# Kernel optimization log

Measured on AMD Instinct MI355X. Metric: run time of the kernel, lower is better.

Reference implementation:

```python
import jax, jax.numpy as jnp
import numpy as np

B, P, C, D, H = 32, 2048, 19, 512, 4
DH = D // H  # 128
EPS = 1e-5


def setup_inputs() -> dict:
    key = jax.random.key(0)
    ks = jax.random.split(key, 12)
    s = 0.02
    return {
        "x": jax.random.normal(ks[0], (B, P, D), jnp.float32),
        "channel_embeddings": jax.random.normal(ks[1], (C, D), jnp.float32),
        "Wq": jax.random.normal(ks[2], (D, D), jnp.float32) * s,
        "bq": jnp.zeros((D,), jnp.float32),
        "Wk": jax.random.normal(ks[3], (D, D), jnp.float32) * s,
        "bk": jnp.zeros((D,), jnp.float32),
        "Wv": jax.random.normal(ks[4], (D, D), jnp.float32) * s,
        "bv": jnp.zeros((D,), jnp.float32),
        "Wo": jax.random.normal(ks[5], (D, D), jnp.float32) * s,
        "bo": jnp.zeros((D,), jnp.float32),
        "gamma": jnp.ones((D,), jnp.float32),
        "beta": jnp.zeros((D,), jnp.float32),
    }


def reference(x, channel_embeddings, Wq, bq, Wk, bk, Wv, bv, Wo, bo, gamma, beta):
    # q: (B, P, H, DH)
    q = (x @ Wq.T + bq).reshape(B, P, H, DH)
    # K/V depend only on channel embeddings (same for every batch/patch in the
    # original; it merely materialized the broadcast). Compute once: (C, H, DH)
    k = (channel_embeddings @ Wk.T + bk).reshape(C, H, DH)
    v = (channel_embeddings @ Wv.T + bv).reshape(C, H, DH)
    # scores over channels: (B, P, C, H)
    scores = jnp.einsum("bphd,chd->bpch", q, k) / jnp.sqrt(jnp.float32(DH))
    weights = jax.nn.softmax(scores, axis=2)  # softmax over channel dim
    # weighted sum of channel values: (B, P, H, DH) -> (B, P, D)
    attended = jnp.einsum("bpch,chd->bphd", weights, v).reshape(B, P, D)
    out = attended @ Wo.T + bo  # dropout is identity in eval mode
    # residual + layernorm
    h = x + out
    mean = jnp.mean(h, axis=-1, keepdims=True)
    var = jnp.mean(jnp.square(h - mean), axis=-1, keepdims=True)
    return (h - mean) * jax.lax.rsqrt(var + EPS) * gamma + beta
```

## Files before the change

### kernel.cpp

```cpp
#include <hip/hip_runtime.h>
#include <hip/hip_bf16.h>

#define C_  19
#define D_  512
#define H_  4
#define DH_ 128
#define NROW 65536
#define CHP_ 96

typedef float f32x4 __attribute__((ext_vector_type(4)));
typedef short bf16x8 __attribute__((ext_vector_type(8)));

__device__ __forceinline__ unsigned short f2bf(float f) {
  union { __hip_bfloat16 h; unsigned short s; } u;
  u.h = __float2bfloat16(f);
  return u.s;
}
__device__ __forceinline__ float bf2f(unsigned short h) {
  return __uint_as_float(((unsigned int)h) << 16);
}
__device__ __forceinline__ bf16x8 ld_cvt8(const float* p) {
  f32x4 v0 = *(const f32x4*)p;
  f32x4 v1 = *(const f32x4*)(p + 4);
  bf16x8 a;
  a[0]=(short)f2bf(v0[0]); a[1]=(short)f2bf(v0[1]);
  a[2]=(short)f2bf(v0[2]); a[3]=(short)f2bf(v0[3]);
  a[4]=(short)f2bf(v1[0]); a[5]=(short)f2bf(v1[1]);
  a[6]=(short)f2bf(v1[2]); a[7]=(short)f2bf(v1[3]);
  return a;
}

__global__ __launch_bounds__(512) void prep(
    const float* __restrict__ ce,
    const float* __restrict__ Wq, const float* __restrict__ bq,
    const float* __restrict__ Wk, const float* __restrict__ bk,
    const float* __restrict__ Wv, const float* __restrict__ bv,
    const float* __restrict__ Wo, const float* __restrict__ bo,
    unsigned short* __restrict__ Mtf, unsigned short* __restrict__ Utf,
    float* __restrict__ s0g)
{
  __shared__ float KV[2][DH_];
  __shared__ float KVp[512];

  const int p = blockIdx.x;
  const int m = threadIdx.x;
  const int mt_off = (p>>4)*8192 + (m>>5)*512 + ((((m>>3)&3)<<4) + (p&15))*8 + (m&7);
  const int ut_off = ((m>>4)*3 + (p>>5))*512 + ((((p>>3)&3)<<4) + (m&15))*8 + (p&7);
  const int c = p >> 2, h = p & 3;

  if (c >= C_) {
    if (p < 80) { Mtf[mt_off] = 0; if (m == 0) s0g[p] = 0.f; }
    Utf[ut_off] = (p == 80) ? f2bf(bo[m]) : (unsigned short)0;
    return;
  }

  {
    const int which = m >> 8;
    const int dh    = (m >> 1) & 127;
    const int half  = m & 1;
    const float* w = (which ? Wv : Wk) + (size_t)(h*DH_ + dh)*D_ + half*256;
    const float* e = ce + (size_t)c*D_ + half*256;
    float acc = 0.f;
    #pragma unroll 8
    for (int d = 0; d < 256; ++d) acc = fmaf(e[d], w[d], acc);
    KVp[m] = acc;
  }
  __syncthreads();
  if (m < 256) {
    const int which = m >> 7, dh = m & 127;
    KV[which][dh] = KVp[2*m] + KVp[2*m+1] + (which ? bv : bk)[h*DH_ + dh];
  }
  __syncthreads();

  const float rs128 = 0.08838834764831843f;
  float macc = 0.f;
  #pragma unroll 4
  for (int dh = 0; dh < DH_; ++dh)
    macc = fmaf(Wq[(size_t)(h*DH_+dh)*D_ + m], KV[0][dh], macc);
  Mtf[mt_off] = f2bf(macc * rs128);

  float uacc = 0.f;
  const float* wor = Wo + (size_t)m*D_ + h*DH_;
  #pragma unroll 4
  for (int dh = 0; dh < DH_; ++dh)
    uacc = fmaf(wor[dh], KV[1][dh], uacc);
  Utf[ut_off] = f2bf(uacc);

  if (m == 0) {
    float sa = 0.f;
    for (int dh = 0; dh < DH_; ++dh) sa = fmaf(bq[h*DH_+dh], KV[0][dh], sa);
    s0g[p] = sa * rs128;
  }
}

__global__ __launch_bounds__(64, 2) void fused16w(
    const float* __restrict__ x,
    const unsigned short* __restrict__ Mtf,
    const unsigned short* __restrict__ Utf,
    const float* __restrict__ s0g,
    const float* __restrict__ gamma, const float* __restrict__ beta,
    float* __restrict__ out)
{
  __shared__ __attribute__((aligned(16))) unsigned short Xbf[16*512];
  __shared__ __attribute__((aligned(16))) unsigned short WaL[16][104];

  const int lane = threadIdx.x;
  const int lhi  = lane >> 4;
  const int llo  = lane & 15;
  const int row0 = blockIdx.x * 16;

  #pragma unroll
  for (int j = 0; j < 16; ++j) {
    bf16x8 a = ld_cvt8(x + (size_t)(row0 + j)*D_ + lane*8);
    int byteoff = j*1024 + ((lane*16) ^ ((j & 7) << 4));
    *(bf16x8*)((char*)Xbf + byteoff) = a;
  }
  asm volatile("s_waitcnt lgkmcnt(0)" ::: "memory");
  __builtin_amdgcn_sched_barrier(0);

  {
    const char* xb = (const char*)Xbf + llo*1024;
    const int swz = (llo & 7) << 4;
    f32x4 acc0 = (f32x4){0,0,0,0}, acc1 = acc0, acc2 = acc0, acc3 = acc0, acc4 = acc0;
    #pragma unroll
    for (int ks = 0; ks < 16; ++ks) {
      bf16x8 a = *(const bf16x8*)(xb + ((ks*64 + lhi*16) ^ swz));
      acc0 = __builtin_amdgcn_mfma_f32_16x16x32_bf16(a, *(const bf16x8*)(Mtf + 0*8192 + ks*512 + lane*8), acc0, 0, 0, 0);
      acc1 = __builtin_amdgcn_mfma_f32_16x16x32_bf16(a, *(const bf16x8*)(Mtf + 1*8192 + ks*512 + lane*8), acc1, 0, 0, 0);
      acc2 = __builtin_amdgcn_mfma_f32_16x16x32_bf16(a, *(const bf16x8*)(Mtf + 2*8192 + ks*512 + lane*8), acc2, 0, 0, 0);
      acc3 = __builtin_amdgcn_mfma_f32_16x16x32_bf16(a, *(const bf16x8*)(Mtf + 3*8192 + ks*512 + lane*8), acc3, 0, 0, 0);
      acc4 = __builtin_amdgcn_mfma_f32_16x16x32_bf16(a, *(const bf16x8*)(Mtf + 4*8192 + ks*512 + lane*8), acc4, 0, 0, 0);
    }
    const bool dead = (llo >= 12);
    float s0v0 = s0g[llo], s0v1 = s0g[16+llo], s0v2 = s0g[32+llo],
          s0v3 = s0g[48+llo], s0v4 = s0g[64+llo];
    #pragma unroll
    for (int r = 0; r < 4; ++r) {
      float v0 = acc0[r] + s0v0;
      float v1 = acc1[r] + s0v1;
      float v2 = acc2[r] + s0v2;
      float v3 = acc3[r] + s0v3;
      float v4 = dead ? -1e30f : (acc4[r] + s0v4);
      float mx = fmaxf(fmaxf(fmaxf(v0, v1), fmaxf(v2, v3)), v4);
      mx = fmaxf(mx, __shfl_xor(mx, 4, 64));
      mx = fmaxf(mx, __shfl_xor(mx, 8, 64));
      float e0 = __expf(v0 - mx), e1 = __expf(v1 - mx), e2 = __expf(v2 - mx),
            e3 = __expf(v3 - mx), e4 = dead ? 0.f : __expf(v4 - mx);
      float sm = e0 + e1 + e2 + e3 + e4;
      sm += __shfl_xor(sm, 4, 64);
      sm += __shfl_xor(sm, 8, 64);
      float inv = 1.f / sm;
      int lr = lhi*4 + r;
      WaL[lr][     llo] = f2bf(e0 * inv);
      WaL[lr][16 + llo] = f2bf(e1 * inv);
      WaL[lr][32 + llo] = f2bf(e2 * inv);
      WaL[lr][48 + llo] = f2bf(e3 * inv);
      WaL[lr][64 + llo] = f2bf(e4 * inv);
    }
    {
      int prow = lhi*4 + (llo & 3);
      int cj   = llo >> 2;
      unsigned short v0 = (cj == 0) ? (unsigned short)0x3F80 : (unsigned short)0;
      WaL[prow][80 + cj*4 + 0] = v0;
      WaL[prow][80 + cj*4 + 1] = 0;
      WaL[prow][80 + cj*4 + 2] = 0;
      WaL[prow][80 + cj*4 + 3] = 0;
    }
  }
  asm volatile("s_waitcnt lgkmcnt(0)" ::: "memory");
  __builtin_amdgcn_sched_barrier(0);

  f32x4 oacc[32];
  #pragma unroll
  for (int i = 0; i < 32; ++i) oacc[i] = (f32x4){0.f,0.f,0.f,0.f};
  #pragma unroll
  for (int ks = 0; ks < 3; ++ks) {
    bf16x8 a = *(const bf16x8*)&WaL[llo][ks*32 + lhi*8];
    #pragma unroll
    for (int t = 0; t < 32; ++t) {
      bf16x8 b = *(const bf16x8*)(Utf + (size_t)(t*3 + ks)*512 + lane*8);
      oacc[t] = __builtin_amdgcn_mfma_f32_16x16x32_bf16(a, b, oacc[t], 0, 0, 0);
    }
  }

  float s[4] = {0,0,0,0}, q[4] = {0,0,0,0};
  #pragma unroll
  for (int t = 0; t < 32; ++t) {
    int n = t*16 + llo;
    #pragma unroll
    for (int r = 0; r < 4; ++r) {
      int mr = lhi*4 + r;
      float xres = bf2f(*(const unsigned short*)
          ((const char*)Xbf + mr*1024 + ((n*2) ^ ((mr & 7) << 4))));
      float val = oacc[t][r] + xres;
      oacc[t][r] = val;
      s[r] += val;
      q[r] = fmaf(val, val, q[r]);
    }
  }
  #pragma unroll
  for (int r = 0; r < 4; ++r) {
    #pragma unroll
    for (int off = 1; off < 16; off <<= 1) {
      s[r] += __shfl_xor(s[r], off, 64);
      q[r] += __shfl_xor(q[r], off, 64);
    }
  }
  float mu_r[4], rstd_r[4];
  #pragma unroll
  for (int r = 0; r < 4; ++r) {
    float mu  = s[r] * (1.f/(float)D_);
    float var = q[r] * (1.f/(float)D_) - mu*mu;
    mu_r[r]   = mu;
    rstd_r[r] = rsqrtf(var + 1e-5f);
  }
  #pragma unroll
  for (int t = 0; t < 32; ++t) {
    int n = t*16 + llo;
    float g = gamma[n], bt = beta[n];
    #pragma unroll
    for (int r = 0; r < 4; ++r) {
      out[(size_t)(row0 + lhi*4 + r)*D_ + n] = (oacc[t][r] - mu_r[r]) * rstd_r[r] * g + bt;
    }
  }
}

extern "C" void kernel_launch(void* const* d_in, const int* in_sizes, int n_in,
                              void* d_out, int out_size, void* d_ws, size_t ws_size,
                              hipStream_t stream) {
  const float* x     = (const float*)d_in[0];
  const float* ce    = (const float*)d_in[1];
  const float* Wq    = (const float*)d_in[2];
  const float* bq    = (const float*)d_in[3];
  const float* Wk    = (const float*)d_in[4];
  const float* bk    = (const float*)d_in[5];
  const float* Wv    = (const float*)d_in[6];
  const float* bv    = (const float*)d_in[7];
  const float* Wo    = (const float*)d_in[8];
  const float* bo    = (const float*)d_in[9];
  const float* gamma = (const float*)d_in[10];
  const float* beta  = (const float*)d_in[11];
  float* out = (float*)d_out;

  char* ws = (char*)d_ws;
  unsigned short* Mtf = (unsigned short*)(ws);
  unsigned short* Utf = (unsigned short*)(ws + 81920);
  float* s0g          = (float*)(ws + 180224);

  prep<<<CHP_, 512, 0, stream>>>(ce, Wq, bq, Wk, bk, Wv, bv, Wo, bo,
                                 Mtf, Utf, s0g);
  fused16w<<<NROW/16, 64, 0, stream>>>(x, Mtf, Utf, s0g, gamma, beta, out);
}
```

Baseline: 140.1 us.

## Restructure fused kernel into 256-row blocks with LDS-staged Utf and transposed score MFMA

Each block now handles 256 rows with 8 waves, and Utf is staged once per block into LDS. The score GEMM is transposed so x is read straight from global into registers, with each wave covering 32 rows. The residual is re-read from global memory in fp32 instead of the bf16 LDS copy. This aims to cut repeated global loads of Utf and raise per-block reuse, but it uses about 150KB of LDS per block, which limits occupancy. The second x read may add memory traffic if it misses cache.

```diff
diff --git a/kernel.cpp b/kernel.cpp
--- a/kernel.cpp
+++ b/kernel.cpp
@@ -7,6 +7,7 @@
 #define DH_ 128
 #define NROW 65536
 #define CHP_ 96
+#define WPITCH 104
 
 typedef float f32x4 __attribute__((ext_vector_type(4)));
 typedef short bf16x8 __attribute__((ext_vector_type(8)));
@@ -15,9 +16,6 @@
   union { __hip_bfloat16 h; unsigned short s; } u;
   u.h = __float2bfloat16(f);
   return u.s;
-}
-__device__ __forceinline__ float bf2f(unsigned short h) {
-  return __uint_as_float(((unsigned int)h) << 16);
 }
 __device__ __forceinline__ bf16x8 ld_cvt8(const float* p) {
   f32x4 v0 = *(const f32x4*)p;
@@ -93,7 +91,7 @@
   }
 }
 
-__global__ __launch_bounds__(64, 2) void fused16w(
+__global__ __launch_bounds__(512, 2) void fused256(
     const float* __restrict__ x,
     const unsigned short* __restrict__ Mtf,
     const unsigned short* __restrict__ Utf,
@@ -101,126 +99,136 @@
     const float* __restrict__ gamma, const float* __restrict__ beta,
     float* __restrict__ out)
 {
-  __shared__ __attribute__((aligned(16))) unsigned short Xbf[16*512];
-  __shared__ __attribute__((aligned(16))) unsigned short WaL[16][104];
-
-  const int lane = threadIdx.x;
+  __shared__ __attribute__((aligned(16))) unsigned short UtfL[CHP_*512];
+  __shared__ __attribute__((aligned(16))) unsigned short WaL[256][WPITCH];
+
+  const int t    = threadIdx.x;
+  const int w    = t >> 6;
+  const int lane = t & 63;
   const int lhi  = lane >> 4;
   const int llo  = lane & 15;
-  const int row0 = blockIdx.x * 16;
+  const int row0 = blockIdx.x * 256;
+  const int wr   = w * 32;
 
   #pragma unroll
-  for (int j = 0; j < 16; ++j) {
-    bf16x8 a = ld_cvt8(x + (size_t)(row0 + j)*D_ + lane*8);
-    int byteoff = j*1024 + ((lane*16) ^ ((j & 7) << 4));
-    *(bf16x8*)((char*)Xbf + byteoff) = a;
-  }
-  asm volatile("s_waitcnt lgkmcnt(0)" ::: "memory");
-  __builtin_amdgcn_sched_barrier(0);
-
+  for (int i = 0; i < 12; ++i) {
+    int off = i*8192 + t*16;
+    *(bf16x8*)((char*)UtfL + off) = *(const bf16x8*)((const char*)Utf + off);
+  }
+
+  f32x4 acc[5][2];
+  #pragma unroll
+  for (int m = 0; m < 5; ++m)
+    #pragma unroll
+    for (int j = 0; j < 2; ++j) acc[m][j] = (f32x4){0,0,0,0};
   {
-    const char* xb = (const char*)Xbf + llo*1024;
-    const int swz = (llo & 7) << 4;
-    f32x4 acc0 = (f32x4){0,0,0,0}, acc1 = acc0, acc2 = acc0, acc3 = acc0, acc4 = acc0;
+    const float* xr0 = x + (size_t)(row0 + wr      + llo)*D_ + lhi*8;
+    const float* xr1 = x + (size_t)(row0 + wr + 16 + llo)*D_ + lhi*8;
     #pragma unroll
     for (int ks = 0; ks < 16; ++ks) {
-      bf16x8 a = *(const bf16x8*)(xb + ((ks*64 + lhi*16) ^ swz));
-      acc0 = __builtin_amdgcn_mfma_f32_16x16x32_bf16(a, *(const bf16x8*)(Mtf + 0*8192 + ks*512 + lane*8), acc0, 0, 0, 0);
-      acc1 = __builtin_amdgcn_mfma_f32_16x16x32_bf16(a, *(const bf16x8*)(Mtf + 1*8192 + ks*512 + lane*8), acc1, 0, 0, 0);
-      acc2 = __builtin_amdgcn_mfma_f32_16x16x32_bf16(a, *(const bf16x8*)(Mtf + 2*8192 + ks*512 + lane*8), acc2, 0, 0, 0);
-      acc3 = __builtin_amdgcn_mfma_f32_16x16x32_bf16(a, *(const bf16x8*)(Mtf + 3*8192 + ks*512 + lane*8), acc3, 0, 0, 0);
-      acc4 = __builtin_amdgcn_mfma_f32_16x16x32_bf16(a, *(const bf16x8*)(Mtf + 4*8192 + ks*512 + lane*8), acc4, 0, 0, 0);
-    }
-    const bool dead = (llo >= 12);
-    float s0v0 = s0g[llo], s0v1 = s0g[16+llo], s0v2 = s0g[32+llo],
-          s0v3 = s0g[48+llo], s0v4 = s0g[64+llo];
+      bf16x8 xb0 = ld_cvt8(xr0 + ks*32);
+      bf16x8 xb1 = ld_cvt8(xr1 + ks*32);
+      #pragma unroll
+      for (int m = 0; m < 5; ++m) {
+        bf16x8 a = *(const bf16x8*)(Mtf + m*8192 + ks*512 + lane*8);
+        acc[m][0] = __builtin_amdgcn_mfma_f32_16x16x32_bf16(a, xb0, acc[m][0], 0, 0, 0);
+        acc[m][1] = __builtin_amdgcn_mfma_f32_16x16x32_bf16(a, xb1, acc[m][1], 0, 0, 0);
+      }
+    }
+  }
+
+  {
+    const bool dead = (lhi == 3);
+    #pragma unroll
+    for (int t2 = 0; t2 < 2; ++t2) {
+      #pragma unroll
+      for (int r = 0; r < 4; ++r) {
+        float v0 = acc[0][t2][r] + s0g[ 0 + lhi*4 + r];
+        float v1 = acc[1][t2][r] + s0g[16 + lhi*4 + r];
+        float v2 = acc[2][t2][r] + s0g[32 + lhi*4 + r];
+        float v3 = acc[3][t2][r] + s0g[48 + lhi*4 + r];
+        float v4 = dead ? -1e30f : (acc[4][t2][r] + s0g[64 + lhi*4 + r]);
+        float mx = fmaxf(fmaxf(fmaxf(v0, v1), fmaxf(v2, v3)), v4);
+        mx = fmaxf(mx, __shfl_xor(mx, 16, 64));
+        mx = fmaxf(mx, __shfl_xor(mx, 32, 64));
+        float e0 = __expf(v0 - mx), e1 = __expf(v1 - mx), e2 = __expf(v2 - mx),
+              e3 = __expf(v3 - mx), e4 = dead ? 0.f : __expf(v4 - mx);
+        float sm = e0 + e1 + e2 + e3 + e4;
+        sm += __shfl_xor(sm, 16, 64);
+        sm += __shfl_xor(sm, 32, 64);
+        float inv = 1.f / sm;
+        int xr = wr + t2*16 + llo;
+        WaL[xr][ 0 + lhi*4 + r] = f2bf(e0 * inv);
+        WaL[xr][16 + lhi*4 + r] = f2bf(e1 * inv);
+        WaL[xr][32 + lhi*4 + r] = f2bf(e2 * inv);
+        WaL[xr][48 + lhi*4 + r] = f2bf(e3 * inv);
+        WaL[xr][64 + lhi*4 + r] = f2bf(e4 * inv);
+      }
+    }
+    {
+      int rr = wr + (lane & 31);
+      int cb = 80 + (lane >> 5) * 8;
+      bf16x8 z = (bf16x8){0,0,0,0,0,0,0,0};
+      if (cb == 80) z[0] = (short)0x3F80;
+      *(bf16x8*)&WaL[rr][cb] = z;
+    }
+  }
+  __syncthreads();
+
+  #pragma unroll 1
+  for (int pp = 0; pp < 2; ++pp) {
+    const int base = wr + pp*16;
+    f32x4 oacc[32];
+    #pragma unroll
+    for (int i = 0; i < 32; ++i) oacc[i] = (f32x4){0,0,0,0};
+    #pragma unroll
+    for (int ks = 0; ks < 3; ++ks) {
+      bf16x8 a = *(const bf16x8*)&WaL[base + llo][ks*32 + lhi*8];
+      #pragma unroll
+      for (int tl = 0; tl < 32; ++tl) {
+        bf16x8 b = *(const bf16x8*)((const char*)UtfL + (size_t)(tl*3 + ks)*1024 + lane*16);
+        oacc[tl] = __builtin_amdgcn_mfma_f32_16x16x32_bf16(a, b, oacc[tl], 0, 0, 0);
+      }
+    }
+
+    float s[4] = {0,0,0,0}, q[4] = {0,0,0,0};
+    #pragma unroll
+    for (int tl = 0; tl < 32; ++tl) {
+      int n = tl*16 + llo;
+      #pragma unroll
+      for (int r = 0; r < 4; ++r) {
+        int mr = base + lhi*4 + r;
+        float val = oacc[tl][r] + x[(size_t)(row0 + mr)*D_ + n];
+        oacc[tl][r] = val;
+        s[r] += val;
+        q[r] = fmaf(val, val, q[r]);
+      }
+    }
     #pragma unroll
     for (int r = 0; r < 4; ++r) {
-      float v0 = acc0[r] + s0v0;
-      float v1 = acc1[r] + s0v1;
-      float v2 = acc2[r] + s0v2;
-      float v3 = acc3[r] + s0v3;
-      float v4 = dead ? -1e30f : (acc4[r] + s0v4);
-      float mx = fmaxf(fmaxf(fmaxf(v0, v1), fmaxf(v2, v3)), v4);
-      mx = fmaxf(mx, __shfl_xor(mx, 4, 64));
-      mx = fmaxf(mx, __shfl_xor(mx, 8, 64));
-      float e0 = __expf(v0 - mx), e1 = __expf(v1 - mx), e2 = __expf(v2 - mx),
-            e3 = __expf(v3 - mx), e4 = dead ? 0.f : __expf(v4 - mx);
-      float sm = e0 + e1 + e2 + e3 + e4;
-      sm += __shfl_xor(sm, 4, 64);
-      sm += __shfl_xor(sm, 8, 64);
-      float inv = 1.f / sm;
-      int lr = lhi*4 + r;
-      WaL[lr][     llo] = f2bf(e0 * inv);
-      WaL[lr][16 + llo] = f2bf(e1 * inv);
-      WaL[lr][32 + llo] = f2bf(e2 * inv);
-      WaL[lr][48 + llo] = f2bf(e3 * inv);
-      WaL[lr][64 + llo] = f2bf(e4 * inv);
-    }
-    {
-      int prow = lhi*4 + (llo & 3);
-      int cj   = llo >> 2;
-      unsigned short v0 = (cj == 0) ? (unsigned short)0x3F80 : (unsigned short)0;
-      WaL[prow][80 + cj*4 + 0] = v0;
-      WaL[prow][80 + cj*4 + 1] = 0;
-      WaL[prow][80 + cj*4 + 2] = 0;
-      WaL[prow][80 + cj*4 + 3] = 0;
-    }
-  }
-  asm volatile("s_waitcnt lgkmcnt(0)" ::: "memory");
-  __builtin_amdgcn_sched_barrier(0);
-
-  f32x4 oacc[32];
-  #pragma unroll
-  for (int i = 0; i < 32; ++i) oacc[i] = (f32x4){0.f,0.f,0.f,0.f};
-  #pragma unroll
-  for (int ks = 0; ks < 3; ++ks) {
-    bf16x8 a = *(const bf16x8*)&WaL[llo][ks*32 + lhi*8];
-    #pragma unroll
-    for (int t = 0; t < 32; ++t) {
-      bf16x8 b = *(const bf16x8*)(Utf + (size_t)(t*3 + ks)*512 + lane*8);
-      oacc[t] = __builtin_amdgcn_mfma_f32_16x16x32_bf16(a, b, oacc[t], 0, 0, 0);
-    }
-  }
-
-  float s[4] = {0,0,0,0}, q[4] = {0,0,0,0};
-  #pragma unroll
-  for (int t = 0; t < 32; ++t) {
-    int n = t*16 + llo;
+      #pragma unroll
+      for (int off = 1; off < 16; off <<= 1) {
+        s[r] += __shfl_xor(s[r], off, 64);
+        q[r] += __shfl_xor(q[r], off, 64);
+      }
+    }
+    float mu_r[4], rstd_r[4];
     #pragma unroll
     for (int r = 0; r < 4; ++r) {
-      int mr = lhi*4 + r;
-      float xres = bf2f(*(const unsigned short*)
-          ((const char*)Xbf + mr*1024 + ((n*2) ^ ((mr & 7) << 4))));
-      float val = oacc[t][r] + xres;
-      oacc[t][r] = val;
-      s[r] += val;
-      q[r] = fmaf(val, val, q[r]);
-    }
-  }
-  #pragma unroll
-  for (int r = 0; r < 4; ++r) {
-    #pragma unroll
-    for (int off = 1; off < 16; off <<= 1) {
-      s[r] += __shfl_xor(s[r], off, 64);
-      q[r] += __shfl_xor(q[r], off, 64);
-    }
-  }
-  float mu_r[4], rstd_r[4];
-  #pragma unroll
-  for (int r = 0; r < 4; ++r) {
-    float mu  = s[r] * (1.f/(float)D_);
-    float var = q[r] * (1.f/(float)D_) - mu*mu;
-    mu_r[r]   = mu;
-    rstd_r[r] = rsqrtf(var + 1e-5f);
-  }
-  #pragma unroll
-  for (int t = 0; t < 32; ++t) {
-    int n = t*16 + llo;
-    float g = gamma[n], bt = beta[n];
-    #pragma unroll
-    for (int r = 0; r < 4; ++r) {
-      out[(size_t)(row0 + lhi*4 + r)*D_ + n] = (oacc[t][r] - mu_r[r]) * rstd_r[r] * g + bt;
+      float mu  = s[r] * (1.f/(float)D_);
+      float var = q[r] * (1.f/(float)D_) - mu*mu;
+      mu_r[r]   = mu;
+      rstd_r[r] = rsqrtf(var + 1e-5f);
+    }
+    #pragma unroll
+    for (int tl = 0; tl < 32; ++tl) {
+      int n = tl*16 + llo;
+      float g = gamma[n], bt = beta[n];
+      #pragma unroll
+      for (int r = 0; r < 4; ++r) {
+        int mr = base + lhi*4 + r;
+        out[(size_t)(row0 + mr)*D_ + n] = (oacc[tl][r] - mu_r[r]) * rstd_r[r] * g + bt;
+      }
     }
   }
 }
@@ -249,5 +257,5 @@
 
   prep<<<CHP_, 512, 0, stream>>>(ce, Wq, bq, Wk, bk, Wv, bv, Wo, bo,
                                  Mtf, Utf, s0g);
-  fused16w<<<NROW/16, 64, 0, stream>>>(x, Mtf, Utf, s0g, gamma, beta, out);
-}
+  fused256<<<NROW/256, 512, 0, stream>>>(x, Mtf, Utf, s0g, gamma, beta, out);
+}
```

After: 156.8 us. +12.0%, slower.

## Drop LDS x staging, split output GEMM into halves to raise occupancy

Applied to the files above, without the earlier changes.

Removes the 16 KB LDS staging of x and loads the MFMA A-operand straight from global memory, converting to bf16 in registers. The output GEMM is split into two 256-column halves, and the first half's residual-added values are stashed in registers as packed bf16. This halves the accumulator register footprint so the launch bound can allow 4 waves per SIMD instead of 2. In exchange, x is read from global twice (projection and residual), and the first half's pre-LayerNorm values lose precision through bf16 packing.

```diff
diff --git a/kernel.cpp b/kernel.cpp
--- a/kernel.cpp
+++ b/kernel.cpp
@@ -93,7 +93,7 @@
   }
 }
 
-__global__ __launch_bounds__(64, 2) void fused16w(
+__global__ __launch_bounds__(64, 4) void fused16s(
     const float* __restrict__ x,
     const unsigned short* __restrict__ Mtf,
     const unsigned short* __restrict__ Utf,
@@ -101,7 +101,6 @@
     const float* __restrict__ gamma, const float* __restrict__ beta,
     float* __restrict__ out)
 {
-  __shared__ __attribute__((aligned(16))) unsigned short Xbf[16*512];
   __shared__ __attribute__((aligned(16))) unsigned short WaL[16][104];
 
   const int lane = threadIdx.x;
@@ -109,22 +108,12 @@
   const int llo  = lane & 15;
   const int row0 = blockIdx.x * 16;
 
-  #pragma unroll
-  for (int j = 0; j < 16; ++j) {
-    bf16x8 a = ld_cvt8(x + (size_t)(row0 + j)*D_ + lane*8);
-    int byteoff = j*1024 + ((lane*16) ^ ((j & 7) << 4));
-    *(bf16x8*)((char*)Xbf + byteoff) = a;
-  }
-  asm volatile("s_waitcnt lgkmcnt(0)" ::: "memory");
-  __builtin_amdgcn_sched_barrier(0);
-
   {
-    const char* xb = (const char*)Xbf + llo*1024;
-    const int swz = (llo & 7) << 4;
     f32x4 acc0 = (f32x4){0,0,0,0}, acc1 = acc0, acc2 = acc0, acc3 = acc0, acc4 = acc0;
+    const float* xr = x + (size_t)(row0 + llo)*D_ + lhi*8;
     #pragma unroll
     for (int ks = 0; ks < 16; ++ks) {
-      bf16x8 a = *(const bf16x8*)(xb + ((ks*64 + lhi*16) ^ swz));
+      bf16x8 a = ld_cvt8(xr + ks*32);
       acc0 = __builtin_amdgcn_mfma_f32_16x16x32_bf16(a, *(const bf16x8*)(Mtf + 0*8192 + ks*512 + lane*8), acc0, 0, 0, 0);
       acc1 = __builtin_amdgcn_mfma_f32_16x16x32_bf16(a, *(const bf16x8*)(Mtf + 1*8192 + ks*512 + lane*8), acc1, 0, 0, 0);
       acc2 = __builtin_amdgcn_mfma_f32_16x16x32_bf16(a, *(const bf16x8*)(Mtf + 2*8192 + ks*512 + lane*8), acc2, 0, 0, 0);
@@ -160,8 +149,7 @@
     {
       int prow = lhi*4 + (llo & 3);
       int cj   = llo >> 2;
-      unsigned short v0 = (cj == 0) ? (unsigned short)0x3F80 : (unsigned short)0;
-      WaL[prow][80 + cj*4 + 0] = v0;
+      WaL[prow][80 + cj*4 + 0] = (cj == 0) ? (unsigned short)0x3F80 : (unsigned short)0;
       WaL[prow][80 + cj*4 + 1] = 0;
       WaL[prow][80 + cj*4 + 2] = 0;
       WaL[prow][80 + cj*4 + 3] = 0;
@@ -170,34 +158,59 @@
   asm volatile("s_waitcnt lgkmcnt(0)" ::: "memory");
   __builtin_amdgcn_sched_barrier(0);
 
-  f32x4 oacc[32];
-  #pragma unroll
-  for (int i = 0; i < 32; ++i) oacc[i] = (f32x4){0.f,0.f,0.f,0.f};
+  float s[4] = {0,0,0,0}, q[4] = {0,0,0,0};
+  unsigned int pk[32];
+  f32x4 oa[16];
+
+  #pragma unroll
+  for (int i = 0; i < 16; ++i) oa[i] = (f32x4){0,0,0,0};
   #pragma unroll
   for (int ks = 0; ks < 3; ++ks) {
-    bf16x8 a = *(const bf16x8*)&WaL[llo][ks*32 + lhi*8];
-    #pragma unroll
-    for (int t = 0; t < 32; ++t) {
-      bf16x8 b = *(const bf16x8*)(Utf + (size_t)(t*3 + ks)*512 + lane*8);
-      oacc[t] = __builtin_amdgcn_mfma_f32_16x16x32_bf16(a, b, oacc[t], 0, 0, 0);
-    }
-  }
-
-  float s[4] = {0,0,0,0}, q[4] = {0,0,0,0};
-  #pragma unroll
-  for (int t = 0; t < 32; ++t) {
-    int n = t*16 + llo;
+    bf16x8 aw = *(const bf16x8*)&WaL[llo][ks*32 + lhi*8];
+    #pragma unroll
+    for (int tl = 0; tl < 16; ++tl) {
+      bf16x8 b = *(const bf16x8*)(Utf + (size_t)(tl*3 + ks)*512 + lane*8);
+      oa[tl] = __builtin_amdgcn_mfma_f32_16x16x32_bf16(aw, b, oa[tl], 0, 0, 0);
+    }
+  }
+  #pragma unroll
+  for (int tl = 0; tl < 16; ++tl) {
+    int n = tl*16 + llo;
     #pragma unroll
     for (int r = 0; r < 4; ++r) {
-      int mr = lhi*4 + r;
-      float xres = bf2f(*(const unsigned short*)
-          ((const char*)Xbf + mr*1024 + ((n*2) ^ ((mr & 7) << 4))));
-      float val = oacc[t][r] + xres;
-      oacc[t][r] = val;
+      float val = oa[tl][r] + x[(size_t)(row0 + lhi*4 + r)*D_ + n];
+      oa[tl][r] = val;
       s[r] += val;
       q[r] = fmaf(val, val, q[r]);
     }
-  }
+    pk[tl*2    ] = (unsigned int)f2bf(oa[tl][0]) | ((unsigned int)f2bf(oa[tl][1]) << 16);
+    pk[tl*2 + 1] = (unsigned int)f2bf(oa[tl][2]) | ((unsigned int)f2bf(oa[tl][3]) << 16);
+  }
+
+  #pragma unroll
+  for (int i = 0; i < 16; ++i) oa[i] = (f32x4){0,0,0,0};
+  #pragma unroll
+  for (int ks = 0; ks < 3; ++ks) {
+    bf16x8 aw = *(const bf16x8*)&WaL[llo][ks*32 + lhi*8];
+    #pragma unroll
+    for (int tl = 0; tl < 16; ++tl) {
+      bf16x8 b = *(const bf16x8*)(Utf + (size_t)((16 + tl)*3 + ks)*512 + lane*8);
+      oa[tl] = __builtin_amdgcn_mfma_f32_16x16x32_bf16(aw, b, oa[tl], 0, 0, 0);
+    }
+  }
+  #pragma unroll
+  for (int tl = 0; tl < 16; ++tl) {
+    int n = 256 + tl*16 + llo;
+    #pragma unroll
+    for (int r = 0; r < 4; ++r) {
+      float val = oa[tl][r] + x[(size_t)(row0 + lhi*4 + r)*D_ + n];
+      oa[tl][r] = val;
+      s[r] += val;
+      q[r] = fmaf(val, val, q[r]);
+    }
+  }
+
+  float mu_r[4], rstd_r[4];
   #pragma unroll
   for (int r = 0; r < 4; ++r) {
     #pragma unroll
@@ -205,23 +218,33 @@
       s[r] += __shfl_xor(s[r], off, 64);
       q[r] += __shfl_xor(q[r], off, 64);
     }
-  }
-  float mu_r[4], rstd_r[4];
-  #pragma unroll
-  for (int r = 0; r < 4; ++r) {
     float mu  = s[r] * (1.f/(float)D_);
     float var = q[r] * (1.f/(float)D_) - mu*mu;
     mu_r[r]   = mu;
     rstd_r[r] = rsqrtf(var + 1e-5f);
   }
-  #pragma unroll
-  for (int t = 0; t < 32; ++t) {
-    int n = t*16 + llo;
+
+  #pragma unroll
+  for (int tl = 0; tl < 16; ++tl) {
+    int n = 256 + tl*16 + llo;
     float g = gamma[n], bt = beta[n];
     #pragma unroll
-    for (int r = 0; r < 4; ++r) {
-      out[(size_t)(row0 + lhi*4 + r)*D_ + n] = (oacc[t][r] - mu_r[r]) * rstd_r[r] * g + bt;
-    }
+    for (int r = 0; r < 4; ++r)
+      out[(size_t)(row0 + lhi*4 + r)*D_ + n] = (oa[tl][r] - mu_r[r]) * rstd_r[r] * g + bt;
+  }
+  #pragma unroll
+  for (int tl = 0; tl < 16; ++tl) {
+    int n = tl*16 + llo;
+    float g = gamma[n], bt = beta[n];
+    float v0 = bf2f((unsigned short)(pk[tl*2    ] & 0xFFFF));
+    float v1 = bf2f((unsigned short)(pk[tl*2    ] >> 16));
+    float v2 = bf2f((unsigned short)(pk[tl*2 + 1] & 0xFFFF));
+    float v3 = bf2f((unsigned short)(pk[tl*2 + 1] >> 16));
+    const size_t ro = (size_t)(row0 + lhi*4)*D_ + n;
+    out[ro        ] = (v0 - mu_r[0]) * rstd_r[0] * g + bt;
+    out[ro +   D_ ] = (v1 - mu_r[1]) * rstd_r[1] * g + bt;
+    out[ro + 2*D_ ] = (v2 - mu_r[2]) * rstd_r[2] * g + bt;
+    out[ro + 3*D_ ] = (v3 - mu_r[3]) * rstd_r[3] * g + bt;
   }
 }
 
@@ -249,5 +272,5 @@
 
   prep<<<CHP_, 512, 0, stream>>>(ce, Wq, bq, Wk, bk, Wv, bv, Wo, bo,
                                  Mtf, Utf, s0g);
-  fused16w<<<NROW/16, 64, 0, stream>>>(x, Mtf, Utf, s0g, gamma, beta, out);
-}
+  fused16s<<<NROW/16, 64, 0, stream>>>(x, Mtf, Utf, s0g, gamma, beta, out);
+}
```

Result: slower. 263.9 us (+88.4%).
